# Performance work log

Hardware: AMD Instinct MI355X
Metric: run time of the kernel (lower is better)

## Reference

```python
import jax, jax.numpy as jnp
from jax import lax
import numpy as np

WIN = 7            # skimage structural_similarity default win_size
K1, K2 = 0.01, 0.03
DATA_RANGE = 1.0


def _mean_filter_valid(x, win):
    k = jnp.ones((1, 1, win, win), x.dtype) / (win * win)
    y = lax.conv_general_dilated(x[:, None], k, (1, 1), 'VALID')
    return y[:, 0]


def ssim_loss(img1, img2):
    # img1, img2: (B, H, W); skimage-style SSIM, mean over batch of (1 - ssim)
    f = lambda z: _mean_filter_valid(z, WIN)
    NP = WIN * WIN
    cov_norm = NP / (NP - 1.0)  # unbiased estimator, as in skimage
    ux, uy = f(img1), f(img2)
    uxx, uyy, uxy = f(img1 * img1), f(img2 * img2), f(img1 * img2)
    vx = cov_norm * (uxx - ux * ux)
    vy = cov_norm * (uyy - uy * uy)
    vxy = cov_norm * (uxy - ux * uy)
    C1 = (K1 * DATA_RANGE) ** 2
    C2 = (K2 * DATA_RANGE) ** 2
    S = ((2 * ux * uy + C1) * (2 * vxy + C2)) / ((ux * ux + uy * uy + C1) * (vx + vy + C2))
    return jnp.mean(1.0 - jnp.mean(S, axis=(1, 2)))


def conv2d_same(x, w, b):
    # x: (B, Cin, H, W), w: (Cout, Cin, 3, 3)
    y = lax.conv_general_dilated(x, w, (1, 1), 'SAME')
    return y + b[None, :, None, None]


def maxpool2(x):
    return lax.reduce_window(x, -jnp.inf, lax.max, (1, 1, 2, 2), (1, 1, 2, 2), 'VALID')


def features(x, w1, b1, w2, b2, w3, b3, w4, b4):
    h = jax.nn.relu(conv2d_same(x, w1, b1))
    h = jax.nn.relu(conv2d_same(h, w2, b2))
    h = maxpool2(h)
    h = jax.nn.relu(conv2d_same(h, w3, b3))
    h = jax.nn.relu(conv2d_same(h, w4, b4))
    return h


def _conv_init(key, cout, cin, k=3):
    # torch Conv2d default init: U(-s, s), s = 1/sqrt(cin*k*k)
    kw, kb = jax.random.split(key)
    s = 1.0 / np.sqrt(cin * k * k)
    w = jax.random.uniform(kw, (cout, cin, k, k), jnp.float32, -s, s)
    b = jax.random.uniform(kb, (cout,), jnp.float32, -s, s)
    return w, b


def setup_inputs() -> dict:
    key = jax.random.key(0)
    ks = jax.random.split(key, 6)
    B, H, W = 8, 256, 256
    sr = jax.random.uniform(ks[0], (B, 1, H, W), jnp.float32)
    hr = jax.random.uniform(ks[1], (B, 1, H, W), jnp.float32)
    w1, b1 = _conv_init(ks[2], 64, 1)
    w2, b2 = _conv_init(ks[3], 128, 64)
    w3, b3 = _conv_init(ks[4], 256, 128)
    w4, b4 = _conv_init(ks[5], 256, 256)
    return {"sr": sr, "hr": hr, "w1": w1, "b1": b1, "w2": w2, "b2": b2,
            "w3": w3, "b3": b3, "w4": w4, "b4": b4}


def reference(sr, hr, w1, b1, w2, b2, w3, b3, w4, b4):
    mse_weight, ssim_weight, perceptual_weight = 1.0, 0.5, 0.1
    mse = jnp.mean((sr - hr) ** 2)
    # torch detaches before SSIM (numpy round-trip) -> no gradient through SSIM
    ssim_l = ssim_loss(lax.stop_gradient(sr[:, 0]), lax.stop_gradient(hr[:, 0]))
    sr_f = features(sr, w1, b1, w2, b2, w3, b3, w4, b4)
    hr_f = features(hr, w1, b1, w2, b2, w3, b3, w4, b4)
    perceptual = jnp.mean((sr_f - hr_f) ** 2)
    total = mse_weight * mse + ssim_weight * ssim_l + perceptual_weight * perceptual
    return total, mse, ssim_l, perceptual
```

## Files before the change

### kernel.cpp

```cpp
#include <hip/hip_runtime.h>
#include <hip/hip_bf16.h>

typedef __hip_bfloat16 bf16;
typedef unsigned char u8;
typedef __attribute__((ext_vector_type(4))) float f32x4;
typedef __attribute__((ext_vector_type(2))) float f32x2;
typedef __attribute__((ext_vector_type(4))) unsigned short us4;
typedef __attribute__((ext_vector_type(8))) int i32x8;
typedef __attribute__((ext_vector_type(4))) unsigned int u32x4;

struct L4 { long a, b, c, d; };
struct U2 { u32x4 x, y; };

__device__ inline unsigned short f2bf(float f) {
    __hip_bfloat16 h = __float2bfloat16(f);
    return __builtin_bit_cast(unsigned short, h);
}

typedef __attribute__((address_space(3))) unsigned int lds_uint;
typedef __attribute__((address_space(1))) const unsigned int g_uint;
__device__ inline void gload_lds16(const void* g, void* l) {
    __builtin_amdgcn_global_load_lds((g_uint*)g, (lds_uint*)l, 16, 0, 0);
}

__device__ inline void block_reduce_atomic(float v, float* dst) {
    #pragma unroll
    for (int o = 32; o > 0; o >>= 1) v += __shfl_down(v, o, 64);
    __shared__ float ws[8];
    const int lane = threadIdx.x & 63;
    const int wid  = threadIdx.x >> 6;
    if (lane == 0) ws[wid] = v;
    __syncthreads();
    if (threadIdx.x == 0) {
        float s = 0.f;
        const int nw = (blockDim.x + 63) >> 6;
        for (int i = 0; i < nw; ++i) s += ws[i];
        atomicAdd(dst, s);
    }
}

__global__ void prep_kernel(const float* __restrict__ w2, u8* __restrict__ wb2,
                            const float* __restrict__ w3, u8* __restrict__ wb3,
                            const float* __restrict__ w4, u8* __restrict__ wb4,
                            float* accs, float* zbuf) {
    int blk = blockIdx.x;
    if (blk == 0) {
        if (threadIdx.x < 8)  accs[threadIdx.x] = 0.f;
        if (threadIdx.x < 64) zbuf[threadIdx.x] = 0.f;
        return;
    }
    const float* w; u8* wb; int CIN, CO, idx;
    if (blk <= 288)       { w = w2; wb = wb2; CIN = 64;  CO = 128; idx = (blk - 1) * 256 + threadIdx.x; }
    else if (blk <= 1440) { w = w3; wb = wb3; CIN = 128; CO = 256; idx = (blk - 289) * 256 + threadIdx.x; }
    else                  { w = w4; wb = wb4; CIN = 256; CO = 256; idx = (blk - 1441) * 256 + threadIdx.x; }
    int n = CO * 9 * CIN;
    if (idx >= n) return;
    int t = idx % 9;
    int rest = idx / 9;
    int ci = rest % CIN;
    int co = rest / CIN;
    float v = w[idx];
    int p = ci >> 5, c32 = ci & 31;
    size_t off = (size_t)p * 288 * CO;
    if (t < 8) {
        off += (((size_t)t * 2 + (c32 >> 4)) * CO + co) * 16 + (c32 & 15);
    } else {
        off += 256 * (size_t)CO + (((size_t)(c32 >> 4)) * CO + co) * 16 + (c32 & 15);
    }
    int r = __builtin_amdgcn_cvt_pk_fp8_f32(v, v, 0, false);
    wb[off] = (u8)(r & 0xff);
}

__global__ void loss_kernel(const float* __restrict__ x, const float* __restrict__ y,
                            float* __restrict__ accs) {
    const int blk = blockIdx.x;
    float val = 0.f;
    float* dst;
    if (blk < 1960) {
        dst = accs + 1;
        const int b = blk / 245;
        const int t = (blk - b * 245) * 256 + threadIdx.x;
        if (t < 250 * 250) {
            const int i = t / 250, j = t - (t / 250) * 250;
            const float* xp = x + (size_t)b * 65536;
            const float* yp = y + (size_t)b * 65536;
            float sx = 0.f, sy = 0.f, sxx = 0.f, syy = 0.f, sxy = 0.f;
            #pragma unroll
            for (int dy = 0; dy < 7; ++dy) {
                const float* xr = xp + (size_t)(i + dy) * 256 + j;
                const float* yr = yp + (size_t)(i + dy) * 256 + j;
                #pragma unroll
                for (int dx = 0; dx < 7; ++dx) {
                    float a = xr[dx], c = yr[dx];
                    sx += a; sy += c;
                    sxx += a * a; syy += c * c; sxy += a * c;
                }
            }
            const float inv = 1.f / 49.f;
            const float cn  = 49.f / 48.f;
            float ux = sx * inv, uy = sy * inv;
            float vx  = cn * (sxx * inv - ux * ux);
            float vy  = cn * (syy * inv - uy * uy);
            float vxy = cn * (sxy * inv - ux * uy);
            const float C1 = 1e-4f, C2 = 9e-4f;
            val = ((2.f * ux * uy + C1) * (2.f * vxy + C2)) /
                  ((ux * ux + uy * uy + C1) * (vx + vy + C2));
        }
    } else {
        dst = accs + 0;
        int i = (blk - 1960) * 256 + threadIdx.x;
        float4 a = ((const float4*)x)[i];
        float4 b = ((const float4*)y)[i];
        float d0 = a.x - b.x, d1 = a.y - b.y, d2 = a.z - b.z, d3 = a.w - b.w;
        val = d0 * d0 + d1 * d1 + d2 * d2 + d3 * d3;
    }
    block_reduce_atomic(val, dst);
}

__global__ void finalize_kernel(const float* __restrict__ accs, float* __restrict__ out) {
    if (threadIdx.x == 0) {
        float mse    = accs[0] * (1.f / 524288.f);
        float ssim_l = 1.f - accs[1] * (1.f / 500000.f);
        float perc   = accs[2] * (1.f / 33554432.f);
        out[0] = mse + 0.5f * ssim_l + 0.1f * perc;
        out[1] = mse;
        out[2] = ssim_l;
        out[3] = perc;
    }
}

__global__ __launch_bounds__(256) void conv1_kernel(
    const float* __restrict__ sr, const float* __restrict__ hr, int nb, int b0,
    const float* __restrict__ w, const float* __restrict__ bias,
    u8* __restrict__ out) {
    const int H = 256, W = 256;
    const int img = blockIdx.y;
    const float* in = (img < nb) ? (sr + (size_t)(b0 + img) * 65536)
                                 : (hr + (size_t)(b0 + img - nb) * 65536);
    int px = blockIdx.x * 256 + threadIdx.x;
    int y = px >> 8, x = px & 255;
    float p[9];
    #pragma unroll
    for (int dy = 0; dy < 3; ++dy)
        #pragma unroll
        for (int dx = 0; dx < 3; ++dx) {
            int gy = y + dy - 1, gx = x + dx - 1;
            float v = 0.f;
            if ((unsigned)gy < (unsigned)H && (unsigned)gx < (unsigned)W)
                v = in[(size_t)gy * W + gx];
            p[dy * 3 + dx] = v;
        }
    #pragma unroll
    for (int g = 0; g < 8; ++g) {
        float v[8];
        #pragma unroll
        for (int c = 0; c < 8; ++c) {
            int co = g * 8 + c;
            float a = bias[co];
            #pragma unroll
            for (int k = 0; k < 9; ++k) a += w[co * 9 + k] * p[k];
            v[c] = fmaxf(a, 0.f);
        }
        uint2 o;
        int r;
        r = __builtin_amdgcn_cvt_pk_fp8_f32(v[0], v[1], 0, false);
        o.x = __builtin_amdgcn_cvt_pk_fp8_f32(v[2], v[3], r, true);
        r = __builtin_amdgcn_cvt_pk_fp8_f32(v[4], v[5], 0, false);
        o.y = __builtin_amdgcn_cvt_pk_fp8_f32(v[6], v[7], r, true);
        *(uint2*)(out + (((size_t)img * 8 + g) * 65536 + px) * 8) = o;
    }
}

#define BUF_SZ   32768
#define N_ACT_CH 720
#define N_CHUNK  1872
#define WT_BOFF  11520

template <int CIN, int EPI>
__global__ __launch_bounds__(256, 2) void conv_mx(
    const u8* __restrict__ in,
    const u8* __restrict__ wb,
    const float* __restrict__ bias,
    u8* __restrict__ out,
    int H, int W, int CO,
    const float* __restrict__ zbuf,
    const u8* __restrict__ fref,
    float* __restrict__ pacc) {
    const int tid  = threadIdx.x;
    const int lane = tid & 63;
    const int wn   = tid >> 6;
    const int xl = lane & 15;
    const int kq = lane >> 4;
    const int x0 = blockIdx.x * 16;
    const int y0 = blockIdx.y * 16;
    const int ngrp = CO >> 6;
    const int img = blockIdx.z / ngrp;
    const int co0 = (blockIdx.z - img * ngrp) << 6;

    __shared__ __align__(16) char smem[2 * BUF_SZ];

    f32x4 acc[4][4];
    #pragma unroll
    for (int m = 0; m < 4; ++m)
        #pragma unroll
        for (int n = 0; n < 4; ++n) acc[m][n] = (f32x4){0.f, 0.f, 0.f, 0.f};

    const size_t HW = (size_t)H * W;
    const u8* inp = in + (size_t)img * (CIN >> 3) * HW * 8;

    const char* srcp[8];
    long adv[8];
    #pragma unroll
    for (int i = 0; i < 8; ++i) {
        int c = tid + i * 256;
        srcp[i] = (const char*)zbuf;
        adv[i] = 0;
        if (c < N_ACT_CH) {
            int g = c / 180, r = c - g * 180;
            int row = r / 10, pp = r - row * 10;
            int gy = y0 - 1 + row, colb = x0 - 2 + pp * 2;
            if ((unsigned)gy < (unsigned)H && (unsigned)colb < (unsigned)(W - 1)) {
                srcp[i] = (const char*)(inp + ((size_t)g * HW + (size_t)gy * W + colb) * 8);
                adv[i] = 4 * HW * 8;
            }
        } else if (c < N_CHUNK) {
            int c2 = c - N_ACT_CH;
            size_t o;
            if (c2 < 1024) {
                int gt = c2 >> 6, co = c2 & 63;
                o = ((size_t)gt * CO + co0 + co) * 16;
            } else {
                int c3 = c2 - 1024;
                int q = c3 >> 6, co = c3 & 63;
                o = 256 * (size_t)CO + ((size_t)q * CO + co0 + co) * 16;
            }
            srcp[i] = (const char*)(wb + o);
            adv[i] = 288 * (size_t)CO;
        }
    }

    int mxo[2];
    #pragma unroll
    for (int g = 0; g < 2; ++g) {
        int t = g * 4 + kq;
        int dy = t / 3, dx = t - dy * 3;
        mxo[g] = (dy * 20 + dx) * 8;
    }
    const int abase = ((wn * 4) * 20 + xl + 1) * 8;
    const int awmx  = WT_BOFF + kq * 2048 + xl * 16;
    const int aw8   = WT_BOFF + 16384 + (kq >> 1) * 1024 + xl * 16 + (kq & 1) * 8;
    const int ab8   = kq * 2880 + abase + (2 * 20 + 2) * 8;

    const int P = CIN / 32;

    {
        char* d = smem + tid * 16;
        #pragma unroll
        for (int i = 0; i < 8; ++i) {
            gload_lds16(srcp[i], d + i * 4096);
            srcp[i] += adv[i];
        }
    }

    for (int p = 0; p < P; ++p) {
        __syncthreads();

        if (p + 1 < P) {
            char* d = smem + ((p + 1) & 1) * BUF_SZ + tid * 16;
            #pragma unroll
            for (int i = 0; i < 8; ++i) {
                gload_lds16(srcp[i], d + i * 4096);
                srcp[i] += adv[i];
            }
        }

        const char* base = smem + (p & 1) * BUF_SZ;

        #pragma unroll
        for (int g = 0; g < 2; ++g) {
            i32x8 A[4];
            #pragma unroll
            for (int mt = 0; mt < 4; ++mt) {
                const char* pa = base + awmx + g * 8192 + mt * 256;
                U2 u{*(const u32x4*)pa, *(const u32x4*)(pa + 1024)};
                A[mt] = __builtin_bit_cast(i32x8, u);
            }
            #pragma unroll
            for (int nt = 0; nt < 4; ++nt) {
                const char* pb = base + abase + mxo[g] + nt * 160;
                L4 l{*(const long*)pb, *(const long*)(pb + 2880),
                     *(const long*)(pb + 5760), *(const long*)(pb + 8640)};
                i32x8 B = __builtin_bit_cast(i32x8, l);
                #pragma unroll
                for (int mt = 0; mt < 4; ++mt)
                    acc[mt][nt] = __builtin_amdgcn_mfma_scale_f32_16x16x128_f8f6f4(
                        A[mt], B, acc[mt][nt], 0, 0,
                        0, 0x7F7F7F7F, 0, 0x7F7F7F7F);
            }
        }

        {
            long A8[4], B8[4];
            #pragma unroll
            for (int mt = 0; mt < 4; ++mt)
                A8[mt] = *(const long*)(base + aw8 + mt * 256);
            #pragma unroll
            for (int nt = 0; nt < 4; ++nt)
                B8[nt] = *(const long*)(base + ab8 + nt * 160);
            #pragma unroll
            for (int mt = 0; mt < 4; ++mt)
                #pragma unroll
                for (int nt = 0; nt < 4; ++nt)
                    acc[mt][nt] = __builtin_amdgcn_mfma_f32_16x16x32_fp8_fp8(
                        A8[mt], B8[nt], acc[mt][nt], 0, 0, 0);
        }
    }

    if (EPI == 0) {
        #pragma unroll
        for (int nt = 0; nt < 4; ++nt) {
            const int y = y0 + wn * 4 + nt;
            #pragma unroll
            for (int mt = 0; mt < 4; ++mt) {
                const int cb = co0 + mt * 16 + kq * 4;
                const f32x4 bv = *(const f32x4*)(bias + cb);
                float v[4];
                #pragma unroll
                for (int r = 0; r < 4; ++r) v[r] = fmaxf(acc[mt][nt][r] + bv[r], 0.f);
                int w0 = __builtin_amdgcn_cvt_pk_fp8_f32(v[0], v[1], 0, false);
                w0 = __builtin_amdgcn_cvt_pk_fp8_f32(v[2], v[3], w0, true);
                *(int*)(out + (((size_t)img * (CO >> 3) + (cb >> 3)) * HW +
                               (size_t)y * W + x0 + xl) * 8 + (cb & 7)) = w0;
            }
        }
    } else if (EPI == 1) {
        const int Hp = H >> 1, Wp = W >> 1;
        const size_t HWp = (size_t)Hp * Wp;
        #pragma unroll
        for (int j = 0; j < 2; ++j) {
            const int py = (y0 + wn * 4 + 2 * j) >> 1;
            const int px = (x0 + xl) >> 1;
            #pragma unroll
            for (int mt = 0; mt < 4; ++mt) {
                const int cb = co0 + mt * 16 + kq * 4;
                const f32x4 bv = *(const f32x4*)(bias + cb);
                float v[4];
                #pragma unroll
                for (int r = 0; r < 4; ++r) {
                    float a = acc[mt][2 * j][r] + bv[r];
                    float b = acc[mt][2 * j + 1][r] + bv[r];
                    float m = fmaxf(a, b);
                    m = fmaxf(m, __shfl_xor(m, 1));
                    v[r] = fmaxf(m, 0.f);
                }
                if (!(lane & 1)) {
                    int w0 = __builtin_amdgcn_cvt_pk_fp8_f32(v[0], v[1], 0, false);
                    w0 = __builtin_amdgcn_cvt_pk_fp8_f32(v[2], v[3], w0, true);
                    *(int*)(out + (((size_t)img * (CO >> 3) + (cb >> 3)) * HWp +
                                   (size_t)py * Wp + px) * 8 + (cb & 7)) = w0;
                }
            }
        }
    } else {
        float s = 0.f;
        #pragma unroll
        for (int nt = 0; nt < 4; ++nt) {
            const int y = y0 + wn * 4 + nt;
            #pragma unroll
            for (int mt = 0; mt < 4; ++mt) {
                const int cb = co0 + mt * 16 + kq * 4;
                const f32x4 bv = *(const f32x4*)(bias + cb);
                int f = *(const int*)(fref + (((size_t)img * (CO >> 3) + (cb >> 3)) * HW +
                                              (size_t)y * W + x0 + xl) * 8 + (cb & 7));
                f32x2 flo = __builtin_amdgcn_cvt_pk_f32_fp8(f, false);
                f32x2 fhi = __builtin_amdgcn_cvt_pk_f32_fp8(f, true);
                float fr[4] = {flo[0], flo[1], fhi[0], fhi[1]};
                #pragma unroll
                for (int r = 0; r < 4; ++r) {
                    float v = fmaxf(acc[mt][nt][r] + bv[r], 0.f);
                    float d = fr[r] - v;
                    s += d * d;
                }
            }
        }
        #pragma unroll
        for (int o = 32; o > 0; o >>= 1) s += __shfl_down(s, o, 64);
        __syncthreads();
        if (lane == 0) *(float*)(smem + wn * 4) = s;
        __syncthreads();
        if (tid == 0) {
            float tot = *(float*)(smem) + *(float*)(smem + 4) +
                        *(float*)(smem + 8) + *(float*)(smem + 12);
            atomicAdd(pacc, tot);
        }
    }
}

extern "C" void kernel_launch(void* const* d_in, const int* in_sizes, int n_in,
                              void* d_out, int out_size, void* d_ws, size_t ws_size,
                              hipStream_t stream) {
    const float* sr = (const float*)d_in[0];
    const float* hr = (const float*)d_in[1];
    const float* w1 = (const float*)d_in[2];
    const float* b1 = (const float*)d_in[3];
    const float* w2 = (const float*)d_in[4];
    const float* b2 = (const float*)d_in[5];
    const float* w3 = (const float*)d_in[6];
    const float* b3 = (const float*)d_in[7];
    const float* w4 = (const float*)d_in[8];
    const float* b4 = (const float*)d_in[9];
    float* out = (float*)d_out;

    char* ws = (char*)d_ws;
    size_t off = 0;
    float* accs = (float*)(ws + off); off += 256;
    float* zbuf = (float*)(ws + off); off += 256;
    u8* wb2 = (u8*)(ws + off); off += (size_t)128 * 9 * 64;
    u8* wb3 = (u8*)(ws + off); off += (size_t)256 * 9 * 128;
    u8* wb4 = (u8*)(ws + off); off += (size_t)256 * 9 * 256;
    const size_t fixed = (off + 255) & ~(size_t)255;

    const size_t MB = 1024u * 1024u;
    int nb = 8;
    while (nb > 1 && fixed + (size_t)nb * 14 * MB > ws_size) nb >>= 1;

    u8* A = (u8*)(ws + fixed);
    u8* P = (u8*)(ws + fixed + (size_t)nb * 8 * MB);
    u8* F = (u8*)(ws + fixed + (size_t)nb * 12 * MB);

    prep_kernel<<<3745, 256, 0, stream>>>(w2, wb2, w3, wb3, w4, wb4, accs, zbuf);
    loss_kernel<<<2472, 256, 0, stream>>>(sr, hr, accs);

    for (int b0 = 0; b0 < 8; b0 += nb) {
        const int ni = 2 * nb;
        conv1_kernel<<<dim3(256, ni), 256, 0, stream>>>(sr, hr, nb, b0, w1, b1, A);
        conv_mx<64, 1><<<dim3(16, 16, ni * 2), 256, 0, stream>>>(
            A, wb2, b2, P, 256, 256, 128, zbuf, nullptr, nullptr);
        conv_mx<128, 0><<<dim3(8, 8, ni * 4), 256, 0, stream>>>(
            P, wb3, b3, A, 128, 128, 256, zbuf, nullptr, nullptr);
        conv_mx<256, 0><<<dim3(8, 8, nb * 4), 256, 0, stream>>>(
            A, wb4, b4, F, 128, 128, 256, zbuf, nullptr, nullptr);
        conv_mx<256, 3><<<dim3(8, 8, nb * 4), 256, 0, stream>>>(
            A + (size_t)nb * 4 * MB, wb4, b4, nullptr, 128, 128, 256, zbuf, F, accs + 2);
    }

    finalize_kernel<<<1, 1, 0, stream>>>(accs, out);
}
```

Baseline: 448.3 us.

## Add wide 32x16 tile conv kernel for conv2 and conv3 layers

```diff
diff --git a/kernel.cpp b/kernel.cpp
--- a/kernel.cpp
+++ b/kernel.cpp
@@ -5,17 +5,11 @@
 typedef unsigned char u8;
 typedef __attribute__((ext_vector_type(4))) float f32x4;
 typedef __attribute__((ext_vector_type(2))) float f32x2;
-typedef __attribute__((ext_vector_type(4))) unsigned short us4;
 typedef __attribute__((ext_vector_type(8))) int i32x8;
 typedef __attribute__((ext_vector_type(4))) unsigned int u32x4;
 
 struct L4 { long a, b, c, d; };
 struct U2 { u32x4 x, y; };
-
-__device__ inline unsigned short f2bf(float f) {
-    __hip_bfloat16 h = __float2bfloat16(f);
-    return __builtin_bit_cast(unsigned short, h);
-}
 
 typedef __attribute__((address_space(3))) unsigned int lds_uint;
 typedef __attribute__((address_space(1))) const unsigned int g_uint;
@@ -178,14 +172,11 @@
 
 template <int CIN, int EPI>
 __global__ __launch_bounds__(256, 2) void conv_mx(
-    const u8* __restrict__ in,
-    const u8* __restrict__ wb,
-    const float* __restrict__ bias,
-    u8* __restrict__ out,
+    const u8* __restrict__ in, const u8* __restrict__ wb,
+    const float* __restrict__ bias, u8* __restrict__ out,
     int H, int W, int CO,
     const float* __restrict__ zbuf,
-    const u8* __restrict__ fref,
-    float* __restrict__ pacc) {
+    const u8* __restrict__ fref, float* __restrict__ pacc) {
     const int tid  = threadIdx.x;
     const int lane = tid & 63;
     const int wn   = tid >> 6;
@@ -264,7 +255,6 @@
 
     for (int p = 0; p < P; ++p) {
         __syncthreads();
-
         if (p + 1 < P) {
             char* d = smem + ((p + 1) & 1) * BUF_SZ + tid * 16;
             #pragma unroll
@@ -273,9 +263,7 @@
                 srcp[i] += adv[i];
             }
         }
-
         const char* base = smem + (p & 1) * BUF_SZ;
-
         #pragma unroll
         for (int g = 0; g < 2; ++g) {
             i32x8 A[4];
@@ -298,7 +286,6 @@
                         0, 0x7F7F7F7F, 0, 0x7F7F7F7F);
             }
         }
-
         {
             long A8[4], B8[4];
             #pragma unroll
@@ -331,34 +318,6 @@
                 w0 = __builtin_amdgcn_cvt_pk_fp8_f32(v[2], v[3], w0, true);
                 *(int*)(out + (((size_t)img * (CO >> 3) + (cb >> 3)) * HW +
                                (size_t)y * W + x0 + xl) * 8 + (cb & 7)) = w0;
-            }
-        }
-    } else if (EPI == 1) {
-        const int Hp = H >> 1, Wp = W >> 1;
-        const size_t HWp = (size_t)Hp * Wp;
-        #pragma unroll
-        for (int j = 0; j < 2; ++j) {
-            const int py = (y0 + wn * 4 + 2 * j) >> 1;
-            const int px = (x0 + xl) >> 1;
-            #pragma unroll
-            for (int mt = 0; mt < 4; ++mt) {
-                const int cb = co0 + mt * 16 + kq * 4;
-                const f32x4 bv = *(const f32x4*)(bias + cb);
-                float v[4];
-                #pragma unroll
-                for (int r = 0; r < 4; ++r) {
-                    float a = acc[mt][2 * j][r] + bv[r];
-                    float b = acc[mt][2 * j + 1][r] + bv[r];
-                    float m = fmaxf(a, b);
-                    m = fmaxf(m, __shfl_xor(m, 1));
-                    v[r] = fmaxf(m, 0.f);
-                }
-                if (!(lane & 1)) {
-                    int w0 = __builtin_amdgcn_cvt_pk_fp8_f32(v[0], v[1], 0, false);
-                    w0 = __builtin_amdgcn_cvt_pk_fp8_f32(v[2], v[3], w0, true);
-                    *(int*)(out + (((size_t)img * (CO >> 3) + (cb >> 3)) * HWp +
-                                   (size_t)py * Wp + px) * 8 + (cb & 7)) = w0;
-                }
             }
         }
     } else {
@@ -392,6 +351,191 @@
             float tot = *(float*)(smem) + *(float*)(smem + 4) +
                         *(float*)(smem + 8) + *(float*)(smem + 12);
             atomicAdd(pacc, tot);
+        }
+    }
+}
+
+#define WBUF_SZ   39168
+#define WN_ACT    1296
+#define WN_CHUNK  2448
+#define WWT_BOFF  20736
+
+template <int CIN, int EPI>
+__global__ __launch_bounds__(256) void conv_mxw(
+    const u8* __restrict__ in, const u8* __restrict__ wb,
+    const float* __restrict__ bias, u8* __restrict__ out,
+    int H, int W, int CO,
+    const float* __restrict__ zbuf) {
+    const int tid  = threadIdx.x;
+    const int lane = tid & 63;
+    const int wn   = tid >> 6;
+    const int xl = lane & 15;
+    const int kq = lane >> 4;
+    const int x0 = blockIdx.x * 32;
+    const int y0 = blockIdx.y * 16;
+    const int ngrp = CO >> 6;
+    const int img = blockIdx.z / ngrp;
+    const int co0 = (blockIdx.z - img * ngrp) << 6;
+
+    __shared__ __align__(16) char smem[WBUF_SZ];
+
+    f32x4 acc[4][8];
+    #pragma unroll
+    for (int m = 0; m < 4; ++m)
+        #pragma unroll
+        for (int n = 0; n < 8; ++n) acc[m][n] = (f32x4){0.f, 0.f, 0.f, 0.f};
+
+    const size_t HW = (size_t)H * W;
+    const u8* inp = in + (size_t)img * (CIN >> 3) * HW * 8;
+    const long actAdv = 4 * (long)HW * 8;
+    const long wtAdv  = 288 * (long)CO;
+
+    const char* srcp[10];
+    unsigned am = 0, wm = 0;
+    #pragma unroll
+    for (int i = 0; i < 10; ++i) {
+        int c = tid + i * 256;
+        srcp[i] = (const char*)zbuf;
+        if (c < WN_ACT) {
+            int g = c / 324, r2 = c - g * 324;
+            int row = r2 / 18, cp = r2 - row * 18;
+            int gy = y0 - 1 + row, colb = x0 - 2 + cp * 2;
+            if ((unsigned)gy < (unsigned)H && (unsigned)colb < (unsigned)(W - 1)) {
+                srcp[i] = (const char*)(inp + ((size_t)g * HW + (size_t)gy * W + colb) * 8);
+                am |= 1u << i;
+            }
+        } else if (c < WN_CHUNK) {
+            int c2 = c - WN_ACT;
+            size_t o;
+            if (c2 < 1024) {
+                int gt = c2 >> 6, co = c2 & 63;
+                o = ((size_t)gt * CO + co0 + co) * 16;
+            } else {
+                int c3 = c2 - 1024;
+                int q = c3 >> 6, co = c3 & 63;
+                o = 256 * (size_t)CO + ((size_t)q * CO + co0 + co) * 16;
+            }
+            srcp[i] = (const char*)(wb + o);
+            wm |= 1u << i;
+        }
+    }
+    const bool sl9 = (tid + 2304) < WN_CHUNK;
+
+    int mxo[2];
+    #pragma unroll
+    for (int g = 0; g < 2; ++g) {
+        int t = g * 4 + kq;
+        int dy = t / 3, dx = t - dy * 3;
+        mxo[g] = dy * 288 + dx * 8;
+    }
+    const int abase = (wn * 4) * 288 + (xl + 1) * 8;
+    const int awmx  = WWT_BOFF + kq * 2048 + xl * 16;
+    const int aw8   = WWT_BOFF + 16384 + (kq >> 1) * 1024 + xl * 16 + (kq & 1) * 8;
+    const int ab8   = kq * 5184 + abase + 2 * 288 + 2 * 8;
+
+    const int P = CIN / 32;
+
+    for (int p = 0; p < P; ++p) {
+        if (p) __syncthreads();
+        {
+            char* d = smem + tid * 16;
+            #pragma unroll
+            for (int i = 0; i < 9; ++i) gload_lds16(srcp[i], d + i * 4096);
+            if (sl9) gload_lds16(srcp[9], d + 9 * 4096);
+            #pragma unroll
+            for (int i = 0; i < 10; ++i) {
+                if (am & (1u << i)) srcp[i] += actAdv;
+                else if (wm & (1u << i)) srcp[i] += wtAdv;
+            }
+        }
+        __syncthreads();
+
+        #pragma unroll
+        for (int g = 0; g < 2; ++g) {
+            i32x8 A[4];
+            #pragma unroll
+            for (int mt = 0; mt < 4; ++mt) {
+                const char* pa = smem + awmx + g * 8192 + mt * 256;
+                U2 u{*(const u32x4*)pa, *(const u32x4*)(pa + 1024)};
+                A[mt] = __builtin_bit_cast(i32x8, u);
+            }
+            #pragma unroll
+            for (int nt = 0; nt < 8; ++nt) {
+                const char* pb = smem + abase + mxo[g] + (nt >> 1) * 288 + (nt & 1) * 128;
+                L4 l{*(const long*)pb, *(const long*)(pb + 5184),
+                     *(const long*)(pb + 10368), *(const long*)(pb + 15552)};
+                i32x8 B = __builtin_bit_cast(i32x8, l);
+                #pragma unroll
+                for (int mt = 0; mt < 4; ++mt)
+                    acc[mt][nt] = __builtin_amdgcn_mfma_scale_f32_16x16x128_f8f6f4(
+                        A[mt], B, acc[mt][nt], 0, 0,
+                        0, 0x7F7F7F7F, 0, 0x7F7F7F7F);
+            }
+        }
+        {
+            long A8[4];
+            #pragma unroll
+            for (int mt = 0; mt < 4; ++mt)
+                A8[mt] = *(const long*)(smem + aw8 + mt * 256);
+            #pragma unroll
+            for (int nt = 0; nt < 8; ++nt) {
+                long B8 = *(const long*)(smem + ab8 + (nt >> 1) * 288 + (nt & 1) * 128);
+                #pragma unroll
+                for (int mt = 0; mt < 4; ++mt)
+                    acc[mt][nt] = __builtin_amdgcn_mfma_f32_16x16x32_fp8_fp8(
+                        A8[mt], B8, acc[mt][nt], 0, 0, 0);
+            }
+        }
+    }
+
+    if (EPI == 0) {
+        #pragma unroll
+        for (int nt = 0; nt < 8; ++nt) {
+            const int y = y0 + wn * 4 + (nt >> 1);
+            const int x = x0 + (nt & 1) * 16 + xl;
+            #pragma unroll
+            for (int mt = 0; mt < 4; ++mt) {
+                const int cb = co0 + mt * 16 + kq * 4;
+                const f32x4 bv = *(const f32x4*)(bias + cb);
+                float v[4];
+                #pragma unroll
+                for (int r = 0; r < 4; ++r) v[r] = fmaxf(acc[mt][nt][r] + bv[r], 0.f);
+                int w0 = __builtin_amdgcn_cvt_pk_fp8_f32(v[0], v[1], 0, false);
+                w0 = __builtin_amdgcn_cvt_pk_fp8_f32(v[2], v[3], w0, true);
+                *(int*)(out + (((size_t)img * (CO >> 3) + (cb >> 3)) * HW +
+                               (size_t)y * W + x) * 8 + (cb & 7)) = w0;
+            }
+        }
+    } else {
+        const int Hp = H >> 1, Wp = W >> 1;
+        const size_t HWp = (size_t)Hp * Wp;
+        #pragma unroll
+        for (int j = 0; j < 2; ++j) {
+            const int py = (y0 + wn * 4 + 2 * j) >> 1;
+            #pragma unroll
+            for (int xh = 0; xh < 2; ++xh) {
+                const int px = (x0 + xh * 16 + xl) >> 1;
+                #pragma unroll
+                for (int mt = 0; mt < 4; ++mt) {
+                    const int cb = co0 + mt * 16 + kq * 4;
+                    const f32x4 bv = *(const f32x4*)(bias + cb);
+                    float v[4];
+                    #pragma unroll
+                    for (int r = 0; r < 4; ++r) {
+                        float a = acc[mt][4 * j + xh][r] + bv[r];
+                        float b = acc[mt][4 * j + 2 + xh][r] + bv[r];
+                        float m = fmaxf(a, b);
+                        m = fmaxf(m, __shfl_xor(m, 1));
+                        v[r] = fmaxf(m, 0.f);
+                    }
+                    if (!(lane & 1)) {
+                        int w0 = __builtin_amdgcn_cvt_pk_fp8_f32(v[0], v[1], 0, false);
+                        w0 = __builtin_amdgcn_cvt_pk_fp8_f32(v[2], v[3], w0, true);
+                        *(int*)(out + (((size_t)img * (CO >> 3) + (cb >> 3)) * HWp +
+                                       (size_t)py * Wp + px) * 8 + (cb & 7)) = w0;
+                    }
+                }
+            }
         }
     }
 }
@@ -434,10 +578,10 @@
     for (int b0 = 0; b0 < 8; b0 += nb) {
         const int ni = 2 * nb;
         conv1_kernel<<<dim3(256, ni), 256, 0, stream>>>(sr, hr, nb, b0, w1, b1, A);
-        conv_mx<64, 1><<<dim3(16, 16, ni * 2), 256, 0, stream>>>(
-            A, wb2, b2, P, 256, 256, 128, zbuf, nullptr, nullptr);
-        conv_mx<128, 0><<<dim3(8, 8, ni * 4), 256, 0, stream>>>(
-            P, wb3, b3, A, 128, 128, 256, zbuf, nullptr, nullptr);
+        conv_mxw<64, 1><<<dim3(8, 16, ni * 2), 256, 0, stream>>>(
+            A, wb2, b2, P, 256, 256, 128, zbuf);
+        conv_mxw<128, 0><<<dim3(4, 8, ni * 4), 256, 0, stream>>>(
+            P, wb3, b3, A, 128, 128, 256, zbuf);
         conv_mx<256, 0><<<dim3(8, 8, nb * 4), 256, 0, stream>>>(
             A, wb4, b4, F, 128, 128, 256, zbuf, nullptr, nullptr);
         conv_mx<256, 3><<<dim3(8, 8, nb * 4), 256, 0, stream>>>(
```

Result: slower. 518.7 us (+15.7%).
